# Kernel tuning notes

Hardware: AMD Instinct MI355X
Metric: run time of the kernel (lower is better)

## Reference

```python
import jax, jax.numpy as jnp
import numpy as np

ADIM = 128
VDIM = 64

def setup_inputs() -> dict:
    key = jax.random.key(0)
    ks = jax.random.split(key, 12)
    B, N, E = 4, 10000, 320000
    pos_0 = jax.random.normal(ks[0], (B, N, 3), dtype=jnp.float32)
    pos_1 = jax.random.normal(ks[1], (B, N, 3), dtype=jnp.float32)
    src = jax.random.randint(ks[2], (E,), 0, N, dtype=jnp.int64)
    dst = jax.random.randint(ks[3], (E,), 0, N, dtype=jnp.int64)
    # parameters (torch default inits approximated; randn for VecLinear as in source)
    Wv = jax.random.normal(ks[4], (VDIM, 6), dtype=jnp.float32)
    def lin(k, fan_in, fan_out):
        kw, kb = jax.random.split(k)
        bound = 1.0 / np.sqrt(fan_in)
        W = jax.random.uniform(kw, (fan_out, fan_in), minval=-bound, maxval=bound, dtype=jnp.float32)
        b = jax.random.uniform(kb, (fan_out,), minval=-bound, maxval=bound, dtype=jnp.float32)
        return W, b
    W1, b1 = lin(ks[5], 6, ADIM)
    W2, b2 = lin(ks[6], ADIM, ADIM)
    W3, b3 = lin(ks[7], ADIM, ADIM)
    return {"pos_0": pos_0, "pos_1": pos_1, "src": src, "dst": dst,
            "Wv": Wv, "W1": W1, "b1": b1, "W2": W2, "b2": b2, "W3": W3, "b3": b3}

def _leaky(x):
    return jnp.where(x >= 0, x, 0.2 * x)

def reference(pos_0, pos_1, src, dst, Wv, W1, b1, W2, b2, W3, b3):
    # gather endpoint positions: (B, E, 3)
    p0s = jnp.take(pos_0, src, axis=1)
    p0d = jnp.take(pos_0, dst, axis=1)
    p1s = jnp.take(pos_1, src, axis=1)
    p1d = jnp.take(pos_1, dst, axis=1)
    # 6 relative vectors: (B, E, 6, 3)
    vecs = jnp.stack([p0d - p0s, p1d - p1s, p1s - p0s, p1d - p0d, p1s - p0d, p1d - p0s], axis=2)
    norms = jnp.sqrt(jnp.sum(vecs * vecs, axis=-1))  # (B, E, 6)
    h = _leaky(jnp.einsum('bei,oi->beo', norms, W1) + b1)
    h = _leaky(jnp.einsum('bei,oi->beo', h, W2) + b2)
    a_out = jnp.einsum('bei,oi->beo', h, W3) + b3  # (B, E, ADIM)
    v_out = jnp.einsum('oi,beik->beok', Wv, vecs) / 3  # (B, E, VDIM, 3)
    return (a_out, v_out)
```

## Files before the change

kernel.cpp:

```cpp
#include <hip/hip_runtime.h>

#define NB 4
#define NN 10000
#define NE 320000
#define EPB 128
#define NPAIR (NE / EPB)
#define NBLK (2 * NB * NPAIR)

typedef unsigned int uint;
typedef unsigned short ushort;
typedef __attribute__((ext_vector_type(8))) short short8;
typedef __attribute__((ext_vector_type(4))) float f32x4;

#define WS_W1T 0
#define WS_W2T 8192
#define WS_W3T 40960
#define WS_WVT 73728

static __device__ __forceinline__ ushort f2bf(float f) {
    uint u = __float_as_uint(f);
    u += 0x7fffu + ((u >> 16) & 1u);
    return (ushort)(u >> 16);
}
static __device__ __forceinline__ uint pack2(float a, float b) {
    return (uint)f2bf(a) | ((uint)f2bf(b) << 16);
}
static __device__ __forceinline__ uint cvtpk(float a, float b) {
    uint r;
    asm("v_cvt_pk_bf16_f32 %0, %1, %2" : "=v"(r) : "v"(a), "v"(b));
    return r;
}
static __device__ __forceinline__ short8 u4s8(uint4 v) {
    union { uint4 u; short8 s; } x; x.u = v; return x.s;
}
static __device__ __forceinline__ f32x4 MF(uint4 a, uint4 b, f32x4 c) {
    return __builtin_amdgcn_mfma_f32_16x16x32_bf16(u4s8(a), u4s8(b), c, 0, 0, 0);
}

__global__ void prep_kernel(const float* __restrict__ W1, const float* __restrict__ W2,
                            const float* __restrict__ W3, const float* __restrict__ Wv,
                            unsigned char* __restrict__ ws) {
    int tid = blockIdx.x * blockDim.x + threadIdx.x;
    if (tid < 4096) {
        const float* W = (tid < 2048) ? W2 : W3;
        uint4* dst = (uint4*)(ws + ((tid < 2048) ? WS_W2T : WS_W3T));
        int f = tid & 2047;
        int lane = f & 63, kt = (f >> 6) & 3, mt = (f >> 8) & 7;
        int la = lane >> 4, lm = lane & 15;
        int n = mt * 16 + lm;
        uint w[4];
        #pragma unroll
        for (int jw = 0; jw < 4; ++jw) {
            int j0 = jw * 2, j1 = j0 + 1;
            int k0 = kt * 32 + (j0 >> 2) * 16 + la * 4 + (j0 & 3);
            int k1 = kt * 32 + (j1 >> 2) * 16 + la * 4 + (j1 & 3);
            w[jw] = pack2(W[n * 128 + k0], W[n * 128 + k1]);
        }
        dst[f] = make_uint4(w[0], w[1], w[2], w[3]);
    } else if (tid < 4608) {
        int f = tid - 4096;
        int lane = f & 63, mt = f >> 6;
        int la = lane >> 4, lm = lane & 15;
        int n = mt * 16 + lm;
        uint w[4];
        #pragma unroll
        for (int jw = 0; jw < 4; ++jw) {
            int j0 = jw * 2, j1 = j0 + 1;
            int k0 = (j0 >> 2) * 16 + la * 4 + (j0 & 3);
            int k1 = (j1 >> 2) * 16 + la * 4 + (j1 & 3);
            float f0 = (k0 < 6) ? W1[n * 6 + k0] : 0.f;
            float f1 = (k1 < 6) ? W1[n * 6 + k1] : 0.f;
            w[jw] = pack2(f0, f1);
        }
        ((uint4*)(ws + WS_W1T))[f] = make_uint4(w[0], w[1], w[2], w[3]);
    } else if (tid < 5376) {
        int f = tid - 4608;
        int lane = f & 63, mt = f >> 6;
        int la = lane >> 4, lm = lane & 15;
        int row = mt * 16 + lm;
        int o = row / 3, c = row - o * 3;
        uint w[4];
        #pragma unroll
        for (int jw = 0; jw < 4; ++jw) {
            float vv[2];
            #pragma unroll
            for (int dc = 0; dc < 2; ++dc) {
                int j = jw * 2 + dc;
                int k = (j >> 2) * 16 + la * 4 + (j & 3);
                int i = k / 3, cc = k - i * 3;
                vv[dc] = (k < 18 && cc == c) ? Wv[o * 6 + i] * (1.f / 3.f) : 0.f;
            }
            w[jw] = pack2(vv[0], vv[1]);
        }
        ((uint4*)(ws + WS_WVT))[f] = make_uint4(w[0], w[1], w[2], w[3]);
    }
}

__global__ __launch_bounds__(256, 3)
void edge_kernel(const float* __restrict__ pos0, const float* __restrict__ pos1,
                 const int* __restrict__ src, const int* __restrict__ dstI,
                 const float* __restrict__ b1, const float* __restrict__ b2,
                 const float* __restrict__ b3,
                 const unsigned char* __restrict__ ws, float* __restrict__ out) {
    __shared__ __align__(16) char smem[42496];
    float (*s_pts)[13] = (float(*)[13])smem;

    const int tid = threadIdx.x;
    const int lane = tid & 63;
    const int w = tid >> 6;
    const int lm = lane & 15;
    const int la = lane >> 4;
    const int ew0 = w * 32;
    const int el = ew0 + (lane & 31);
    const int side = lane >> 5;

    const int bid = blockIdx.x;
    const int kind = bid & 1;
    const int idx = bid >> 1;
    const int b = idx / NPAIR;
    const int e0 = (idx % NPAIR) * EPB;
    const size_t eg0 = (size_t)b * NE + e0;

    const f32x4 zero4 = {0.f, 0.f, 0.f, 0.f};

    {
        const int e = e0 + el;
        const int node = side ? dstI[e] : src[e];
        const size_t pb = ((size_t)b * NN + node) * 3;
        float a0 = pos0[pb], a1 = pos0[pb + 1], a2 = pos0[pb + 2];
        float c0 = pos1[pb], c1 = pos1[pb + 1], c2 = pos1[pb + 2];
        s_pts[el][side * 3 + 0] = a0;
        s_pts[el][side * 3 + 1] = a1;
        s_pts[el][side * 3 + 2] = a2;
        s_pts[el][6 + side * 3 + 0] = c0;
        s_pts[el][6 + side * 3 + 1] = c1;
        s_pts[el][6 + side * 3 + 2] = c2;
    }

    if (kind == 0) {
        float (*s_vecs)[20] = (float(*)[20])(smem + 6656);
        {
            float P[12];
            #pragma unroll
            for (int i = 0; i < 12; ++i) P[i] = s_pts[el][i];
            if (side == 0) {
                const int va[4] = {1, 3, 2, 3}, vbx[4] = {0, 2, 0, 1};
                float v[4][3];
                #pragma unroll
                for (int i = 0; i < 4; ++i)
                    #pragma unroll
                    for (int c = 0; c < 3; ++c) v[i][c] = P[va[i] * 3 + c] - P[vbx[i] * 3 + c];
                float4 t0 = {v[0][0], v[0][1], v[0][2], v[1][0]};
                float4 t1 = {v[1][1], v[1][2], v[2][0], v[2][1]};
                float4 t2 = {v[2][2], v[3][0], v[3][1], v[3][2]};
                *(float4*)&s_vecs[el][0] = t0;
                *(float4*)&s_vecs[el][4] = t1;
                *(float4*)&s_vecs[el][8] = t2;
            } else {
                float v4[3], v5[3];
                #pragma unroll
                for (int c = 0; c < 3; ++c) {
                    v4[c] = P[6 + c] - P[3 + c];
                    v5[c] = P[9 + c] - P[0 + c];
                }
                float4 t = {v4[0], v4[1], v4[2], v5[0]};
                *(float4*)&s_vecs[el][12] = t;
                float2 t2 = {v5[1], v5[2]};
                *(float2*)&s_vecs[el][16] = t2;
            }
        }
        uint4 vbv[2];
        #pragma unroll
        for (int nt = 0; nt < 2; ++nt) {
            const int e = ew0 + nt * 16 + lm;
            float4 q = *(const float4*)&s_vecs[e][la * 4];
            uint c2 = 0;
            if (la == 0) c2 = cvtpk(s_vecs[e][16], s_vecs[e][17]);
            vbv[nt] = make_uint4(cvtpk(q.x, q.y), cvtpk(q.z, q.w), c2, 0u);
        }
        const uint4* WVT = (const uint4*)(ws + WS_WVT);
        uint4 wv[12];
        #pragma unroll
        for (int mt = 0; mt < 12; ++mt) wv[mt] = WVT[mt * 64 + lane];
        float* vout = out + (size_t)NB * NE * 128;
        #pragma unroll
        for (int mt = 0; mt < 12; ++mt)
            #pragma unroll
            for (int nt = 0; nt < 2; ++nt) {
                f32x4 av = MF(wv[mt], vbv[nt], zero4);
                const size_t e = eg0 + ew0 + nt * 16 + lm;
                *(f32x4*)&vout[e * 192 + mt * 16 + la * 4] = av;
            }
        return;
    }

    float* s_normf = (float*)(smem + 6656);
    uint4* s_W2 = (uint4*)(smem + 6656 + 3072);

    const uint4* W2T = (const uint4*)(ws + WS_W2T);
    {
        uint4 stg[8];
        #pragma unroll
        for (int it = 0; it < 8; ++it) stg[it] = W2T[it * 256 + tid];
        #pragma unroll
        for (int it = 0; it < 8; ++it) s_W2[it * 256 + tid] = stg[it];
    }

    {
        float P[12];
        #pragma unroll
        for (int i = 0; i < 12; ++i) P[i] = s_pts[el][i];
        if (side == 0) {
            const int va[4] = {1, 3, 2, 3}, vbx[4] = {0, 2, 0, 1};
            #pragma unroll
            for (int i = 0; i < 4; ++i) {
                float x = P[va[i] * 3 + 0] - P[vbx[i] * 3 + 0];
                float y = P[va[i] * 3 + 1] - P[vbx[i] * 3 + 1];
                float z = P[va[i] * 3 + 2] - P[vbx[i] * 3 + 2];
                s_normf[i * 128 + el] = sqrtf(x * x + y * y + z * z);
            }
        } else {
            float x4 = P[6] - P[3], y4 = P[7] - P[4], z4 = P[8] - P[5];
            float x5 = P[9] - P[0], y5 = P[10] - P[1], z5 = P[11] - P[2];
            s_normf[4 * 128 + el] = sqrtf(x4 * x4 + y4 * y4 + z4 * z4);
            s_normf[5 * 128 + el] = sqrtf(x5 * x5 + y5 * y5 + z5 * z5);
        }
    }
    __syncthreads();

    f32x4 acc[8][2];
    {
        uint4 vb1[2];
        #pragma unroll
        for (int nt = 0; nt < 2; ++nt) {
            const int e = ew0 + nt * 16 + lm;
            uint c0 = 0, c1 = 0;
            if (la == 0) {
                c0 = cvtpk(s_normf[0 * 128 + e], s_normf[1 * 128 + e]);
                c1 = cvtpk(s_normf[2 * 128 + e], s_normf[3 * 128 + e]);
            } else if (la == 1) {
                c0 = cvtpk(s_normf[4 * 128 + e], s_normf[5 * 128 + e]);
            }
            vb1[nt] = make_uint4(c0, c1, 0u, 0u);
        }
        const uint4* W1T = (const uint4*)(ws + WS_W1T);
        uint4 w1f[8];
        #pragma unroll
        for (int mt = 0; mt < 8; ++mt) w1f[mt] = W1T[mt * 64 + lane];
        #pragma unroll
        for (int mt = 0; mt < 8; ++mt)
            #pragma unroll
            for (int nt = 0; nt < 2; ++nt)
                acc[mt][nt] = MF(w1f[mt], vb1[nt], zero4);
    }
    uint4 vb[2][4];
    #pragma unroll
    for (int mt = 0; mt < 8; ++mt) {
        f32x4 bc = *(const f32x4*)&b1[mt * 16 + la * 4];
        #pragma unroll
        for (int nt = 0; nt < 2; ++nt)
            #pragma unroll
            for (int r = 0; r < 4; ++r) {
                float x = acc[mt][nt][r] + bc[r];
                acc[mt][nt][r] = fmaxf(x, 0.2f * x);
            }
    }
    #pragma unroll
    for (int nt = 0; nt < 2; ++nt)
        #pragma unroll
        for (int kt = 0; kt < 4; ++kt)
            vb[nt][kt] = make_uint4(
                cvtpk(acc[2*kt][nt][0], acc[2*kt][nt][1]),
                cvtpk(acc[2*kt][nt][2], acc[2*kt][nt][3]),
                cvtpk(acc[2*kt+1][nt][0], acc[2*kt+1][nt][1]),
                cvtpk(acc[2*kt+1][nt][2], acc[2*kt+1][nt][3]));

    #pragma unroll
    for (int mt = 0; mt < 8; ++mt)
        #pragma unroll
        for (int nt = 0; nt < 2; ++nt) acc[mt][nt] = zero4;
    #pragma unroll
    for (int kt = 0; kt < 4; ++kt) {
        uint4 wf[8];
        #pragma unroll
        for (int mt = 0; mt < 8; ++mt) wf[mt] = s_W2[(mt * 4 + kt) * 64 + lane];
        #pragma unroll
        for (int mt = 0; mt < 8; ++mt)
            #pragma unroll
            for (int nt = 0; nt < 2; ++nt)
                acc[mt][nt] = MF(wf[mt], vb[nt][kt], acc[mt][nt]);
    }
    #pragma unroll
    for (int mt = 0; mt < 8; ++mt) {
        f32x4 bc = *(const f32x4*)&b2[mt * 16 + la * 4];
        #pragma unroll
        for (int nt = 0; nt < 2; ++nt)
            #pragma unroll
            for (int r = 0; r < 4; ++r) {
                float x = acc[mt][nt][r] + bc[r];
                acc[mt][nt][r] = fmaxf(x, 0.2f * x);
            }
    }
    #pragma unroll
    for (int nt = 0; nt < 2; ++nt)
        #pragma unroll
        for (int kt = 0; kt < 4; ++kt)
            vb[nt][kt] = make_uint4(
                cvtpk(acc[2*kt][nt][0], acc[2*kt][nt][1]),
                cvtpk(acc[2*kt][nt][2], acc[2*kt][nt][3]),
                cvtpk(acc[2*kt+1][nt][0], acc[2*kt+1][nt][1]),
                cvtpk(acc[2*kt+1][nt][2], acc[2*kt+1][nt][3]));

    const uint4* W3T = (const uint4*)(ws + WS_W3T);
    #pragma unroll
    for (int mt = 0; mt < 8; ++mt)
        #pragma unroll
        for (int nt = 0; nt < 2; ++nt) acc[mt][nt] = zero4;
    #pragma unroll
    for (int kt = 0; kt < 4; ++kt) {
        uint4 wf[8];
        #pragma unroll
        for (int mt = 0; mt < 8; ++mt) wf[mt] = W3T[(mt * 4 + kt) * 64 + lane];
        #pragma unroll
        for (int mt = 0; mt < 8; ++mt)
            #pragma unroll
            for (int nt = 0; nt < 2; ++nt)
                acc[mt][nt] = MF(wf[mt], vb[nt][kt], acc[mt][nt]);
    }
    #pragma unroll
    for (int mt = 0; mt < 8; ++mt) {
        f32x4 bc = *(const f32x4*)&b3[mt * 16 + la * 4];
        #pragma unroll
        for (int nt = 0; nt < 2; ++nt) {
            f32x4 v = acc[mt][nt] + bc;
            const size_t e = eg0 + ew0 + nt * 16 + lm;
            *(f32x4*)&out[e * 128 + mt * 16 + la * 4] = v;
        }
    }
}

extern "C" void kernel_launch(void* const* d_in, const int* in_sizes, int n_in,
                              void* d_out, int out_size, void* d_ws, size_t ws_size,
                              hipStream_t stream) {
    const float* pos0 = (const float*)d_in[0];
    const float* pos1 = (const float*)d_in[1];
    const int* src = (const int*)d_in[2];
    const int* dstI = (const int*)d_in[3];
    const float* Wv = (const float*)d_in[4];
    const float* W1 = (const float*)d_in[5];
    const float* b1 = (const float*)d_in[6];
    const float* W2 = (const float*)d_in[7];
    const float* b2 = (const float*)d_in[8];
    const float* W3 = (const float*)d_in[9];
    const float* b3 = (const float*)d_in[10];
    unsigned char* ws = (unsigned char*)d_ws;
    float* out = (float*)d_out;

    prep_kernel<<<dim3(21), dim3(256), 0, stream>>>(W1, W2, W3, Wv, ws);
    edge_kernel<<<dim3(NBLK), dim3(256), 0, stream>>>(pos0, pos1, src, dstI, b1, b2, b3, ws, out);
}
```

Measured before the change: 390.9 us.

## Stage a_out through swizzled LDS for coalesced stores, drop W2 LDS staging

Each wave now writes its 16x128 output tile into a per-wave LDS buffer with an XOR swizzle, then reads it back in row-contiguous order so global stores are fully coalesced 1 KB runs rather than strided 16-byte pieces. The block-wide copy of W2 into shared memory and the __syncthreads are removed, and W2 fragments are read straight from global/L2 like W3. Block indices are remapped so groups of 8 tiles alternate between the vector and MLP kinds, which may change the load balance across CUs. The extra LDS round trip adds latency and some LDS traffic per output tile.

Result: slower. 512.9 us (+31.2%).

```diff
diff --git a/kernel.cpp b/kernel.cpp
--- a/kernel.cpp
+++ b/kernel.cpp
@@ -5,7 +5,8 @@
 #define NE 320000
 #define EPB 128
 #define NPAIR (NE / EPB)
-#define NBLK (2 * NB * NPAIR)
+#define NTIL (NB * NPAIR)
+#define NBLK (2 * NTIL)
 
 typedef unsigned int uint;
 typedef unsigned short ushort;
@@ -102,8 +103,10 @@
                  const float* __restrict__ b1, const float* __restrict__ b2,
                  const float* __restrict__ b3,
                  const unsigned char* __restrict__ ws, float* __restrict__ out) {
-    __shared__ __align__(16) char smem[42496];
-    float (*s_pts)[13] = (float(*)[13])smem;
+    __shared__ __align__(16) float smem[12416];
+    float* s_pts = smem;
+    float* s_vn = smem + 1664;
+    float* s_stage = smem + 1664 + 2560;
 
     const int tid = threadIdx.x;
     const int lane = tid & 63;
@@ -115,34 +118,29 @@
     const int side = lane >> 5;
 
     const int bid = blockIdx.x;
-    const int kind = bid & 1;
-    const int idx = bid >> 1;
+    const int kind = (bid >> 3) & 1;
+    const int idx = ((bid >> 4) << 3) | (bid & 7);
     const int b = idx / NPAIR;
-    const int e0 = (idx % NPAIR) * EPB;
+    const int e0 = (idx - b * NPAIR) * EPB;
     const size_t eg0 = (size_t)b * NE + e0;
-
     const f32x4 zero4 = {0.f, 0.f, 0.f, 0.f};
 
     {
-        const int e = e0 + el;
-        const int node = side ? dstI[e] : src[e];
+        const int node = side ? dstI[e0 + el] : src[e0 + el];
         const size_t pb = ((size_t)b * NN + node) * 3;
-        float a0 = pos0[pb], a1 = pos0[pb + 1], a2 = pos0[pb + 2];
-        float c0 = pos1[pb], c1 = pos1[pb + 1], c2 = pos1[pb + 2];
-        s_pts[el][side * 3 + 0] = a0;
-        s_pts[el][side * 3 + 1] = a1;
-        s_pts[el][side * 3 + 2] = a2;
-        s_pts[el][6 + side * 3 + 0] = c0;
-        s_pts[el][6 + side * 3 + 1] = c1;
-        s_pts[el][6 + side * 3 + 2] = c2;
+        s_pts[el * 13 + side * 3 + 0] = pos0[pb + 0];
+        s_pts[el * 13 + side * 3 + 1] = pos0[pb + 1];
+        s_pts[el * 13 + side * 3 + 2] = pos0[pb + 2];
+        s_pts[el * 13 + 6 + side * 3 + 0] = pos1[pb + 0];
+        s_pts[el * 13 + 6 + side * 3 + 1] = pos1[pb + 1];
+        s_pts[el * 13 + 6 + side * 3 + 2] = pos1[pb + 2];
     }
 
     if (kind == 0) {
-        float (*s_vecs)[20] = (float(*)[20])(smem + 6656);
         {
             float P[12];
             #pragma unroll
-            for (int i = 0; i < 12; ++i) P[i] = s_pts[el][i];
+            for (int i = 0; i < 12; ++i) P[i] = s_pts[el * 13 + i];
             if (side == 0) {
                 const int va[4] = {1, 3, 2, 3}, vbx[4] = {0, 2, 0, 1};
                 float v[4][3];
@@ -150,12 +148,12 @@
                 for (int i = 0; i < 4; ++i)
                     #pragma unroll
                     for (int c = 0; c < 3; ++c) v[i][c] = P[va[i] * 3 + c] - P[vbx[i] * 3 + c];
-                float4 t0 = {v[0][0], v[0][1], v[0][2], v[1][0]};
-                float4 t1 = {v[1][1], v[1][2], v[2][0], v[2][1]};
-                float4 t2 = {v[2][2], v[3][0], v[3][1], v[3][2]};
-                *(float4*)&s_vecs[el][0] = t0;
-                *(float4*)&s_vecs[el][4] = t1;
-                *(float4*)&s_vecs[el][8] = t2;
+                float4 t0v = {v[0][0], v[0][1], v[0][2], v[1][0]};
+                float4 t1v = {v[1][1], v[1][2], v[2][0], v[2][1]};
+                float4 t2v = {v[2][2], v[3][0], v[3][1], v[3][2]};
+                *(float4*)&s_vn[el * 20 + 0] = t0v;
+                *(float4*)&s_vn[el * 20 + 4] = t1v;
+                *(float4*)&s_vn[el * 20 + 8] = t2v;
             } else {
                 float v4[3], v5[3];
                 #pragma unroll
@@ -163,53 +161,41 @@
                     v4[c] = P[6 + c] - P[3 + c];
                     v5[c] = P[9 + c] - P[0 + c];
                 }
-                float4 t = {v4[0], v4[1], v4[2], v5[0]};
-                *(float4*)&s_vecs[el][12] = t;
-                float2 t2 = {v5[1], v5[2]};
-                *(float2*)&s_vecs[el][16] = t2;
+                float4 tv4 = {v4[0], v4[1], v4[2], v5[0]};
+                *(float4*)&s_vn[el * 20 + 12] = tv4;
+                float2 tv2 = {v5[1], v5[2]};
+                *(float2*)&s_vn[el * 20 + 16] = tv2;
             }
         }
         uint4 vbv[2];
         #pragma unroll
         for (int nt = 0; nt < 2; ++nt) {
             const int e = ew0 + nt * 16 + lm;
-            float4 q = *(const float4*)&s_vecs[e][la * 4];
+            float4 q = *(const float4*)&s_vn[e * 20 + la * 4];
             uint c2 = 0;
-            if (la == 0) c2 = cvtpk(s_vecs[e][16], s_vecs[e][17]);
+            if (la == 0) c2 = cvtpk(s_vn[e * 20 + 16], s_vn[e * 20 + 17]);
             vbv[nt] = make_uint4(cvtpk(q.x, q.y), cvtpk(q.z, q.w), c2, 0u);
         }
         const uint4* WVT = (const uint4*)(ws + WS_WVT);
         uint4 wv[12];
         #pragma unroll
         for (int mt = 0; mt < 12; ++mt) wv[mt] = WVT[mt * 64 + lane];
-        float* vout = out + (size_t)NB * NE * 128;
+        float* voutP = out + (size_t)NB * NE * 128;
         #pragma unroll
         for (int mt = 0; mt < 12; ++mt)
             #pragma unroll
             for (int nt = 0; nt < 2; ++nt) {
                 f32x4 av = MF(wv[mt], vbv[nt], zero4);
                 const size_t e = eg0 + ew0 + nt * 16 + lm;
-                *(f32x4*)&vout[e * 192 + mt * 16 + la * 4] = av;
+                *(f32x4*)&voutP[e * 192 + mt * 16 + la * 4] = av;
             }
         return;
-    }
-
-    float* s_normf = (float*)(smem + 6656);
-    uint4* s_W2 = (uint4*)(smem + 6656 + 3072);
-
-    const uint4* W2T = (const uint4*)(ws + WS_W2T);
-    {
-        uint4 stg[8];
-        #pragma unroll
-        for (int it = 0; it < 8; ++it) stg[it] = W2T[it * 256 + tid];
-        #pragma unroll
-        for (int it = 0; it < 8; ++it) s_W2[it * 256 + tid] = stg[it];
     }
 
     {
         float P[12];
         #pragma unroll
-        for (int i = 0; i < 12; ++i) P[i] = s_pts[el][i];
+        for (int i = 0; i < 12; ++i) P[i] = s_pts[el * 13 + i];
         if (side == 0) {
             const int va[4] = {1, 3, 2, 3}, vbx[4] = {0, 2, 0, 1};
             #pragma unroll
@@ -217,16 +203,19 @@
                 float x = P[va[i] * 3 + 0] - P[vbx[i] * 3 + 0];
                 float y = P[va[i] * 3 + 1] - P[vbx[i] * 3 + 1];
                 float z = P[va[i] * 3 + 2] - P[vbx[i] * 3 + 2];
-                s_normf[i * 128 + el] = sqrtf(x * x + y * y + z * z);
+                s_vn[i * 128 + el] = sqrtf(x * x + y * y + z * z);
             }
         } else {
             float x4 = P[6] - P[3], y4 = P[7] - P[4], z4 = P[8] - P[5];
             float x5 = P[9] - P[0], y5 = P[10] - P[1], z5 = P[11] - P[2];
-            s_normf[4 * 128 + el] = sqrtf(x4 * x4 + y4 * y4 + z4 * z4);
-            s_normf[5 * 128 + el] = sqrtf(x5 * x5 + y5 * y5 + z5 * z5);
-        }
-    }
-    __syncthreads();
+            s_vn[4 * 128 + el] = sqrtf(x4 * x4 + y4 * y4 + z4 * z4);
+            s_vn[5 * 128 + el] = sqrtf(x5 * x5 + y5 * y5 + z5 * z5);
+        }
+    }
+
+    const uint4* W1T = (const uint4*)(ws + WS_W1T);
+    const uint4* W2T = (const uint4*)(ws + WS_W2T);
+    const uint4* W3T = (const uint4*)(ws + WS_W3T);
 
     f32x4 acc[8][2];
     {
@@ -236,22 +225,20 @@
             const int e = ew0 + nt * 16 + lm;
             uint c0 = 0, c1 = 0;
             if (la == 0) {
-                c0 = cvtpk(s_normf[0 * 128 + e], s_normf[1 * 128 + e]);
-                c1 = cvtpk(s_normf[2 * 128 + e], s_normf[3 * 128 + e]);
+                c0 = cvtpk(s_vn[0 * 128 + e], s_vn[1 * 128 + e]);
+                c1 = cvtpk(s_vn[2 * 128 + e], s_vn[3 * 128 + e]);
             } else if (la == 1) {
-                c0 = cvtpk(s_normf[4 * 128 + e], s_normf[5 * 128 + e]);
+                c0 = cvtpk(s_vn[4 * 128 + e], s_vn[5 * 128 + e]);
             }
             vb1[nt] = make_uint4(c0, c1, 0u, 0u);
         }
-        const uint4* W1T = (const uint4*)(ws + WS_W1T);
-        uint4 w1f[8];
-        #pragma unroll
-        for (int mt = 0; mt < 8; ++mt) w1f[mt] = W1T[mt * 64 + lane];
-        #pragma unroll
-        for (int mt = 0; mt < 8; ++mt)
+        #pragma unroll
+        for (int mt = 0; mt < 8; ++mt) {
+            uint4 w1m = W1T[mt * 64 + lane];
             #pragma unroll
             for (int nt = 0; nt < 2; ++nt)
-                acc[mt][nt] = MF(w1f[mt], vb1[nt], zero4);
+                acc[mt][nt] = MF(w1m, vb1[nt], zero4);
+        }
     }
     uint4 vb[2][4];
     #pragma unroll
@@ -283,7 +270,7 @@
     for (int kt = 0; kt < 4; ++kt) {
         uint4 wf[8];
         #pragma unroll
-        for (int mt = 0; mt < 8; ++mt) wf[mt] = s_W2[(mt * 4 + kt) * 64 + lane];
+        for (int mt = 0; mt < 8; ++mt) wf[mt] = W2T[(mt * 4 + kt) * 64 + lane];
         #pragma unroll
         for (int mt = 0; mt < 8; ++mt)
             #pragma unroll
@@ -311,7 +298,6 @@
                 cvtpk(acc[2*kt+1][nt][0], acc[2*kt+1][nt][1]),
                 cvtpk(acc[2*kt+1][nt][2], acc[2*kt+1][nt][3]));
 
-    const uint4* W3T = (const uint4*)(ws + WS_W3T);
     #pragma unroll
     for (int mt = 0; mt < 8; ++mt)
         #pragma unroll
@@ -327,14 +313,25 @@
             for (int nt = 0; nt < 2; ++nt)
                 acc[mt][nt] = MF(wf[mt], vb[nt][kt], acc[mt][nt]);
     }
-    #pragma unroll
-    for (int mt = 0; mt < 8; ++mt) {
-        f32x4 bc = *(const f32x4*)&b3[mt * 16 + la * 4];
-        #pragma unroll
-        for (int nt = 0; nt < 2; ++nt) {
+
+    float* stg = s_stage + w * 2048;
+    const int sw = (lm & 3) << 4;
+    #pragma unroll
+    for (int nt = 0; nt < 2; ++nt) {
+        #pragma unroll
+        for (int mt = 0; mt < 8; ++mt) {
+            f32x4 bc = *(const f32x4*)&b3[mt * 16 + la * 4];
             f32x4 v = acc[mt][nt] + bc;
-            const size_t e = eg0 + ew0 + nt * 16 + lm;
-            *(f32x4*)&out[e * 128 + mt * 16 + la * 4] = v;
+            *(f32x4*)&stg[lm * 128 + ((mt * 16 + la * 4) ^ sw)] = v;
+        }
+        float* gb = out + (eg0 + ew0 + nt * 16) * 128;
+        #pragma unroll
+        for (int i = 0; i < 8; ++i) {
+            const int flat = i * 256 + lane * 4;
+            const int r = flat >> 7;
+            const int c = flat & 127;
+            f32x4 v = *(const f32x4*)&stg[r * 128 + (c ^ ((r & 3) << 4))];
+            *(f32x4*)&gb[flat] = v;
         }
     }
 }
```
